# Kernel optimization log

Hardware: AMD Instinct MI355X
Metric: run time of the kernel (lower is better)

## Reference

```python
import jax, jax.numpy as jnp
import numpy as np

N, E, D, H, DH, FF, C, L = 50000, 640000, 128, 8, 16, 256, 5, 6
EPS = 1e-5


def _bn(x, g, b):
    # training-mode BatchNorm1d over the node dimension
    m = jnp.mean(x, axis=0)
    v = jnp.var(x, axis=0)
    return (x - m) * jax.lax.rsqrt(v + EPS) * g + b


def _sparse_mha(x, src, dst, Wq, Wk, Wv, Wo):
    # edge-restricted multi-head attention: softmax over incoming edges per dst node
    q = (x @ Wq).reshape(N, H, DH)
    k = (x @ Wk).reshape(N, H, DH)
    v = (x @ Wv).reshape(N, H, DH)
    s = jnp.einsum('ehd,ehd->eh', q[dst], k[src]) * (1.0 / np.sqrt(DH))  # [E,H]
    smax = jax.ops.segment_max(s, dst, num_segments=N)
    smax = jnp.where(jnp.isfinite(smax), smax, 0.0)  # guard isolated nodes
    e = jnp.exp(s - smax[dst])
    den = jax.ops.segment_sum(e, dst, num_segments=N)
    alpha = e / jnp.where(den > 0, den, 1.0)[dst]
    out = jax.ops.segment_sum(alpha[:, :, None] * v[src], dst, num_segments=N)  # [N,H,DH]
    return out.reshape(N, D) @ Wo


def setup_inputs() -> dict:
    key = jax.random.key(0)
    ks = jax.random.split(key, 18)
    f = lambda k, shp, sc: (jax.random.normal(k, shp, jnp.float32) * sc)
    return {
        'x': jax.random.normal(ks[0], (N, D), jnp.float32),
        'edge_index': jax.random.randint(ks[1], (2, E), 0, N),
        'Wq': f(ks[2], (L, D, D), 0.08),
        'Wk': f(ks[3], (L, D, D), 0.08),
        'Wv': f(ks[4], (L, D, D), 0.08),
        'Wo': f(ks[5], (L, D, D), 0.08),
        'g1': jnp.ones((L, D), jnp.float32),
        'bn1': jnp.zeros((L, D), jnp.float32),
        'W1': f(ks[6], (L, D, FF), 0.08),
        'bf1': jnp.zeros((L, FF), jnp.float32),
        'W2': f(ks[7], (L, FF, D), 0.06),
        'bf2': jnp.zeros((L, D), jnp.float32),
        'g2': jnp.ones((L, D), jnp.float32),
        'bn2': jnp.zeros((L, D), jnp.float32),
        'Wp': f(ks[8], (D, C), 0.08),
        'bp': jnp.zeros((C,), jnp.float32),
    }


def reference(x, edge_index, Wq, Wk, Wv, Wo, g1, bn1, W1, bf1, W2, bf2, g2, bn2, Wp, bp):
    src, dst = edge_index[0], edge_index[1]
    for i in range(L):  # fixed small layer count
        res = x  # residual is Identity (num_input == num_output)
        a = _sparse_mha(x, src, dst, Wq[i], Wk[i], Wv[i], Wo[i])
        x = _bn(a + res, g1[i], bn1[i])
        h = jax.nn.relu(x @ W1[i] + bf1[i])  # leakiness=0 -> relu
        x = _bn(x + (h @ W2[i] + bf2[i]), g2[i], bn2[i])
    node_pred = x @ Wp + bp
    return node_pred
```

## Files before the change

kernel.cpp:

```cpp
#include <hip/hip_runtime.h>
#include <hip/hip_bf16.h>
#include <cstdio>

#define NN 50000
#define EE 640000
#define DD 128
#define HH 8
#define DH 16
#define FFD 256
#define CC 5
#define LL 6
#define EPSV 1e-5f

typedef __attribute__((ext_vector_type(8))) short bf16x8;
typedef __attribute__((ext_vector_type(8))) unsigned short ushort8;
typedef __attribute__((ext_vector_type(4))) float f32x4;

__device__ __forceinline__ float bfu2f(unsigned short u) {
  union { unsigned int i; float f; } x; x.i = ((unsigned int)u) << 16; return x.f;
}
__device__ __forceinline__ unsigned short f2bf(float f) {
  union { float f; unsigned int i; } x; x.f = f;
  unsigned int r = (x.i + 0x7fffu + ((x.i >> 16) & 1u)) >> 16;
  return (unsigned short)r;
}

__global__ void detect_kernel(const unsigned int* __restrict__ g1w, int* __restrict__ flag) {
  if (threadIdx.x == 0 && blockIdx.x == 0) *flag = (g1w[0] == 0x3F803F80u) ? 1 : 0;
}

struct ConvJobs { const void* in[8]; float* out[8]; int n[8]; };
__global__ __launch_bounds__(256) void convert_batch_kernel(ConvJobs jobs, const int* __restrict__ flag) {
  int b = blockIdx.x;
  const void* in = jobs.in[b];
  float* out = jobs.out[b];
  int n = jobs.n[b];
  int use_bf = *flag;
  for (int i = threadIdx.x; i < n; i += 256) {
    if (use_bf) out[i] = bfu2f(((const unsigned short*)in)[i]);
    else        out[i] = ((const float*)in)[i];
  }
}

__global__ __launch_bounds__(256) void to_bf16_kernel(const void* __restrict__ in,
                                                      unsigned short* __restrict__ out, int n,
                                                      const int* __restrict__ flag) {
  int i = blockIdx.x * blockDim.x + threadIdx.x;
  if (i >= n) return;
  if (*flag) out[i] = ((const unsigned short*)in)[i];
  else       out[i] = f2bf(((const float*)in)[i]);
}

__global__ __launch_bounds__(256) void t_qkv_kernel(const void* __restrict__ wq, const void* __restrict__ wk,
                                                    const void* __restrict__ wv,
                                                    unsigned short* __restrict__ qkvT,
                                                    const int* __restrict__ flag) {
  int k = blockIdx.x, which = blockIdx.y, l = blockIdx.z;
  const void* in = (which == 0) ? wq : (which == 1) ? wk : wv;
  size_t off = (size_t)l * DD * DD;
  unsigned short* out = qkvT + (size_t)l * 384 * DD + (size_t)which * DD * DD;
  int use_bf = *flag;
  for (int n = threadIdx.x; n < DD; n += 256) {
    unsigned short v;
    if (use_bf) v = ((const unsigned short*)in)[off + (size_t)k * DD + n];
    else        v = f2bf(((const float*)in)[off + (size_t)k * DD + n]);
    out[(size_t)n * DD + k] = v;
  }
}

__global__ __launch_bounds__(256) void t_w_kernel(const void* __restrict__ in,
                                                  unsigned short* __restrict__ out,
                                                  int K, int N, const int* __restrict__ flag) {
  int k = blockIdx.x, l = blockIdx.y;
  size_t off = (size_t)l * K * N;
  unsigned short* o = out + (size_t)l * K * N;
  int use_bf = *flag;
  for (int n = threadIdx.x; n < N; n += 256) {
    unsigned short v;
    if (use_bf) v = ((const unsigned short*)in)[off + (size_t)k * N + n];
    else        v = f2bf(((const float*)in)[off + (size_t)k * N + n]);
    o[(size_t)n * K + k] = v;
  }
}

__global__ __launch_bounds__(256) void zero_kernel(int* __restrict__ p, int n) {
  int i = blockIdx.x * blockDim.x + threadIdx.x;
  if (i < n) p[i] = 0;
}

__global__ __launch_bounds__(256) void count_kernel(const int* __restrict__ dst, int* __restrict__ counts) {
  int e = blockIdx.x * blockDim.x + threadIdx.x;
  if (e < EE) atomicAdd(&counts[dst[e]], 1);
}

__global__ __launch_bounds__(256) void scan1_kernel(const int* __restrict__ counts,
                                                    int* __restrict__ row_ptr, int* __restrict__ partials) {
  __shared__ int sh[256];
  int t = threadIdx.x;
  int i = blockIdx.x * 256 + t;
  int v = (i < NN) ? counts[i] : 0;
  sh[t] = v; __syncthreads();
#pragma unroll
  for (int off = 1; off < 256; off <<= 1) {
    int u = (t >= off) ? sh[t - off] : 0;
    __syncthreads();
    sh[t] += u;
    __syncthreads();
  }
  if (i < NN) row_ptr[i] = sh[t] - v;
  if (t == 255) partials[blockIdx.x] = sh[t];
}

__global__ __launch_bounds__(256) void scan2_kernel(int* __restrict__ partials, int nb) {
  __shared__ int sh[256];
  int t = threadIdx.x;
  int v = (t < nb) ? partials[t] : 0;
  sh[t] = v; __syncthreads();
#pragma unroll
  for (int off = 1; off < 256; off <<= 1) {
    int u = (t >= off) ? sh[t - off] : 0;
    __syncthreads();
    sh[t] += u;
    __syncthreads();
  }
  if (t < nb) partials[t] = sh[t] - v;
}

__global__ __launch_bounds__(256) void scan3_kernel(int* __restrict__ row_ptr, const int* __restrict__ partials) {
  int i = blockIdx.x * 256 + threadIdx.x;
  if (i < NN) row_ptr[i] += partials[blockIdx.x];
  if (i == 0) row_ptr[NN] = EE;
}

__global__ __launch_bounds__(256) void fill_kernel(const int* __restrict__ src, const int* __restrict__ dst,
                                                   const int* __restrict__ row_ptr, int* __restrict__ cursor,
                                                   int* __restrict__ csr_src) {
  int e = blockIdx.x * blockDim.x + threadIdx.x;
  if (e < EE) {
    int d = dst[e];
    int pos = row_ptr[d] + atomicAdd(&cursor[d], 1);
    csr_src[pos] = src[e];
  }
}

template<int K, bool RELU, bool HASBIAS, bool HASRES, bool OUTBF, bool STATS>
__global__ __launch_bounds__(256) void mfma_gemm(const unsigned short* __restrict__ A,
                                                 const unsigned short* __restrict__ BT,
                                                 const float* __restrict__ bias,
                                                 const unsigned short* __restrict__ resid,
                                                 void* __restrict__ C, float* __restrict__ stats,
                                                 int M, int ldc) {
  __shared__ float lsum[64];
  __shared__ float lsq[64];
  int tid = threadIdx.x;
  int lane = tid & 63, wave = tid >> 6;
  int m0 = blockIdx.x * 128 + wave * 32;
  int n0 = blockIdx.y * 64;
  int lm = lane & 15;
  int quad = lane >> 4;
  int kq = quad * 8;

  int rowA[2];
#pragma unroll
  for (int r = 0; r < 2; r++) {
    int rr = m0 + 16 * r + lm;
    rowA[r] = (rr < M) ? rr : (M - 1);
  }
  const unsigned short* aptr0 = A + (size_t)rowA[0] * K + kq;
  const unsigned short* aptr1 = A + (size_t)rowA[1] * K + kq;
  const unsigned short* bptr[4];
#pragma unroll
  for (int c = 0; c < 4; c++)
    bptr[c] = BT + (size_t)(n0 + 16 * c + lm) * K + kq;

  f32x4 acc[2][4];
#pragma unroll
  for (int r = 0; r < 2; r++)
#pragma unroll
    for (int c = 0; c < 4; c++) acc[r][c] = (f32x4){0.f, 0.f, 0.f, 0.f};

#pragma unroll
  for (int kc = 0; kc < K; kc += 128) {
    bf16x8 a[2][4], b[4][4];
#pragma unroll
    for (int ks = 0; ks < 4; ks++) {
      a[0][ks] = *(const bf16x8*)(aptr0 + kc + ks * 32);
      a[1][ks] = *(const bf16x8*)(aptr1 + kc + ks * 32);
    }
#pragma unroll
    for (int c = 0; c < 4; c++)
#pragma unroll
      for (int ks = 0; ks < 4; ks++)
        b[c][ks] = *(const bf16x8*)(bptr[c] + kc + ks * 32);
#pragma unroll
    for (int ks = 0; ks < 4; ks++)
#pragma unroll
      for (int r = 0; r < 2; r++)
#pragma unroll
        for (int c = 0; c < 4; c++)
          acc[r][c] = __builtin_amdgcn_mfma_f32_16x16x32_bf16(b[c][ks], a[r][ks], acc[r][c], 0, 0, 0);
  }

  if (STATS) {
    if (tid < 64) { lsum[tid] = 0.f; lsq[tid] = 0.f; }
    __syncthreads();
  }

  float st_s[4][4], st_q[4][4];
  if (STATS) {
#pragma unroll
    for (int c = 0; c < 4; c++)
#pragma unroll
      for (int reg = 0; reg < 4; reg++) { st_s[c][reg] = 0.f; st_q[c][reg] = 0.f; }
  }

#pragma unroll
  for (int r = 0; r < 2; r++) {
    int row = m0 + 16 * r + lm;
    if (row >= M) continue;
#pragma unroll
    for (int c = 0; c < 4; c++) {
      int col = n0 + 16 * c + quad * 4;
      float4 bv = HASBIAS ? *(const float4*)(bias + col) : make_float4(0.f, 0.f, 0.f, 0.f);
      float o[4];
      o[0] = acc[r][c][0] + bv.x; o[1] = acc[r][c][1] + bv.y;
      o[2] = acc[r][c][2] + bv.z; o[3] = acc[r][c][3] + bv.w;
      if (HASRES) {
        ushort4 rr = *(const ushort4*)(resid + (size_t)row * ldc + col);
        o[0] += bfu2f(rr.x); o[1] += bfu2f(rr.y); o[2] += bfu2f(rr.z); o[3] += bfu2f(rr.w);
      }
      if (RELU) {
        o[0] = fmaxf(o[0], 0.f); o[1] = fmaxf(o[1], 0.f);
        o[2] = fmaxf(o[2], 0.f); o[3] = fmaxf(o[3], 0.f);
      }
      size_t idx = (size_t)row * ldc + col;
      if (OUTBF) {
        ushort4 w;
        w.x = f2bf(o[0]); w.y = f2bf(o[1]); w.z = f2bf(o[2]); w.w = f2bf(o[3]);
        *(ushort4*)((unsigned short*)C + idx) = w;
      } else {
        *(float4*)((float*)C + idx) = make_float4(o[0], o[1], o[2], o[3]);
      }
      if (STATS) {
#pragma unroll
        for (int reg = 0; reg < 4; reg++) {
          st_s[c][reg] += o[reg];
          st_q[c][reg] = fmaf(o[reg], o[reg], st_q[c][reg]);
        }
      }
    }
  }

  if (STATS) {
#pragma unroll
    for (int c = 0; c < 4; c++)
#pragma unroll
      for (int reg = 0; reg < 4; reg++) {
        float s = st_s[c][reg], q = st_q[c][reg];
        s += __shfl_xor(s, 1);  q += __shfl_xor(q, 1);
        s += __shfl_xor(s, 2);  q += __shfl_xor(q, 2);
        s += __shfl_xor(s, 4);  q += __shfl_xor(q, 4);
        s += __shfl_xor(s, 8);  q += __shfl_xor(q, 8);
        if (lm == 0) {
          atomicAdd(&lsum[16 * c + quad * 4 + reg], s);
          atomicAdd(&lsq[16 * c + quad * 4 + reg], q);
        }
      }
    __syncthreads();
    if (tid < 64) {
      atomicAdd(&stats[n0 + tid], lsum[tid]);
      atomicAdd(&stats[128 + n0 + tid], lsq[tid]);
    }
  }
}

__global__ __launch_bounds__(256) void attn_kernel(const unsigned short* __restrict__ qkv,
                                                   const int* __restrict__ row_ptr,
                                                   const int* __restrict__ csr_src,
                                                   unsigned short* __restrict__ t1) {
  int t = blockIdx.x * blockDim.x + threadIdx.x;
  int half = t & 1;
  int nh = t >> 1;
  int n = nh >> 3, h = nh & 7;
  const unsigned short* qp = qkv + (size_t)n * 384 + h * 16 + half * 8;
  float qf[8];
  {
    bf16x8 q0 = *(const bf16x8*)qp;
#pragma unroll
    for (int i = 0; i < 8; i++) qf[i] = bfu2f((unsigned short)q0[i]);
  }
  float m = -3.0e38f, l = 0.f;
  float A[8];
#pragma unroll
  for (int i = 0; i < 8; i++) A[i] = 0.f;
  int e0 = row_ptr[n], e1 = row_ptr[n + 1];
  if (e0 < e1) {
    int s = csr_src[e0];
    const unsigned short* kp = qkv + (size_t)s * 384 + 128 + h * 16 + half * 8;
    bf16x8 k0 = *(const bf16x8*)kp;
    bf16x8 v0 = *(const bf16x8*)(kp + 128);
    for (int e = e0; e < e1; e++) {
      int sn = csr_src[(e + 1 < e1) ? e + 1 : e];
      const unsigned short* kpn = qkv + (size_t)sn * 384 + 128 + h * 16 + half * 8;
      bf16x8 nk0 = *(const bf16x8*)kpn;
      bf16x8 nv0 = *(const bf16x8*)(kpn + 128);

      float part = 0.f;
#pragma unroll
      for (int i = 0; i < 8; i++) part += qf[i] * bfu2f((unsigned short)k0[i]);
      float sc = (part + __shfl_xor(part, 1)) * 0.25f;
      float mn = fmaxf(m, sc);
      float cf = __expf(m - mn);
      float p  = __expf(sc - mn);
      l = l * cf + p;
#pragma unroll
      for (int i = 0; i < 8; i++)
        A[i] = A[i] * cf + p * bfu2f((unsigned short)v0[i]);
      m = mn;
      k0 = nk0; v0 = nv0;
    }
  }
  float inv = (l > 0.f) ? 1.f / l : 0.f;
  ushort8 o0;
#pragma unroll
  for (int i = 0; i < 8; i++) o0[i] = f2bf(A[i] * inv);
  unsigned short* op = t1 + (size_t)n * 128 + h * 16 + half * 8;
  *(ushort8*)op = o0;
}

__global__ __launch_bounds__(256) void bn_apply_kernel(const float4* __restrict__ y4,
                                                       const float* __restrict__ statsL,
                                                       const float* __restrict__ g,
                                                       const float* __restrict__ b,
                                                       ushort4* __restrict__ xb) {
  __shared__ float ssc[128];
  __shared__ float ssh[128];
  int t = threadIdx.x;
  if (t < 128) {
    float mean = statsL[t] * (1.f / NN);
    float var  = statsL[128 + t] * (1.f / NN) - mean * mean;
    var = fmaxf(var, 0.f);
    float sc = g[t] * rsqrtf(var + EPSV);
    ssc[t] = sc;
    ssh[t] = b[t] - mean * sc;
  }
  __syncthreads();
  int i = blockIdx.x * 256 + t;
  const int total = NN * (DD / 4);
  if (i >= total) return;
  int c4 = (i & 31) * 4;
  float4 v = y4[i];
  ushort4 o;
  o.x = f2bf(fmaf(v.x, ssc[c4 + 0], ssh[c4 + 0]));
  o.y = f2bf(fmaf(v.y, ssc[c4 + 1], ssh[c4 + 1]));
  o.z = f2bf(fmaf(v.z, ssc[c4 + 2], ssh[c4 + 2]));
  o.w = f2bf(fmaf(v.w, ssc[c4 + 3], ssh[c4 + 3]));
  xb[i] = o;
}

__global__ __launch_bounds__(256) void proj_kernel(const unsigned short* __restrict__ x,
                                                   const float* __restrict__ Wp,
                                                   const float* __restrict__ bp,
                                                   void* __restrict__ out,
                                                   const int* __restrict__ flag) {
  __shared__ float W[DD * CC];
  __shared__ float bias[CC];
  for (int i = threadIdx.x; i < DD * CC; i += 256) W[i] = Wp[i];
  if (threadIdx.x < CC) bias[threadIdx.x] = bp[threadIdx.x];
  __syncthreads();
  int n = blockIdx.x * blockDim.x + threadIdx.x;
  if (n >= NN) return;
  float acc[CC];
#pragma unroll
  for (int c = 0; c < CC; c++) acc[c] = bias[c];
  const ushort4* xp = (const ushort4*)(x + (size_t)n * DD);
#pragma unroll
  for (int k4 = 0; k4 < DD / 4; k4++) {
    ushort4 u = xp[k4];
    float a0 = bfu2f(u.x), a1 = bfu2f(u.y), a2 = bfu2f(u.z), a3 = bfu2f(u.w);
    const float* w = &W[k4 * 4 * CC];
#pragma unroll
    for (int c = 0; c < CC; c++)
      acc[c] += a0 * w[c] + a1 * w[CC + c] + a2 * w[2 * CC + c] + a3 * w[3 * CC + c];
  }
  if (*flag) {
    __hip_bfloat16* o16 = (__hip_bfloat16*)out;
#pragma unroll
    for (int c = 0; c < CC; c++) o16[(size_t)n * CC + c] = __float2bfloat16(acc[c]);
  } else {
    float* o32 = (float*)out;
#pragma unroll
    for (int c = 0; c < CC; c++) o32[(size_t)n * CC + c] = acc[c];
  }
}

extern "C" void kernel_launch(void* const* d_in, const int* in_sizes, int n_in,
                              void* d_out, int out_size, void* d_ws, size_t ws_size,
                              hipStream_t stream) {
  const int* ei = (const int*)d_in[1];

  char* p = (char*)d_ws;
  auto carve = [&](size_t bytes) { char* r = p; p += (bytes + 255) & ~(size_t)255; return (void*)r; };
  unsigned short* xb   = (unsigned short*)carve((size_t)NN * DD * 2);
  unsigned short* qkv  = (unsigned short*)carve((size_t)NN * 384 * 2);
  unsigned short* t1   = (unsigned short*)carve((size_t)NN * DD * 2);
  unsigned short* hbuf = (unsigned short*)carve((size_t)NN * FFD * 2);
  float* y             = (float*)carve((size_t)NN * DD * 4);
  float* stats = (float*)carve(12 * 256 * 4);
  int* row_ptr = (int*)carve((size_t)(NN + 1) * 4);
  int* cursor  = (int*)carve((size_t)NN * 4);
  int* counts  = (int*)carve((size_t)NN * 4);
  int* csr_src = (int*)carve((size_t)EE * 4);
  int* flag    = (int*)carve(256);
  int* partials = (int*)carve(256 * 4);
  unsigned short* qkvT = (unsigned short*)carve((size_t)LL * 384 * DD * 2);
  unsigned short* WoT  = (unsigned short*)carve((size_t)LL * DD * DD * 2);
  unsigned short* W1T  = (unsigned short*)carve((size_t)LL * FFD * DD * 2);
  unsigned short* W2T  = (unsigned short*)carve((size_t)LL * DD * FFD * 2);
  float* g1_f  = (float*)carve((size_t)LL * DD * 4);
  float* bn1_f = (float*)carve((size_t)LL * DD * 4);
  float* bf1_f = (float*)carve((size_t)LL * FFD * 4);
  float* bf2_f = (float*)carve((size_t)LL * DD * 4);
  float* g2_f  = (float*)carve((size_t)LL * DD * 4);
  float* bn2_f = (float*)carve((size_t)LL * DD * 4);
  float* Wp_f  = (float*)carve((size_t)DD * CC * 4);
  float* bp_f  = (float*)carve((size_t)CC * 4);
  size_t need = (size_t)(p - (char*)d_ws);
  if (need > ws_size) {
    fprintf(stderr, "kernel_launch: workspace too small: need %zu, have %zu\n", need, ws_size);
    return;
  }

  const int* src  = ei;
  const int* dstp = ei + EE;

  detect_kernel<<<1, 64, 0, stream>>>((const unsigned int*)d_in[6], flag);
  to_bf16_kernel<<<(NN * DD + 255) / 256, 256, 0, stream>>>(d_in[0], xb, NN * DD, flag);

  {
    ConvJobs j;
    j.in[0] = d_in[6];  j.out[0] = g1_f;  j.n[0] = LL * DD;
    j.in[1] = d_in[7];  j.out[1] = bn1_f; j.n[1] = LL * DD;
    j.in[2] = d_in[9];  j.out[2] = bf1_f; j.n[2] = LL * FFD;
    j.in[3] = d_in[11]; j.out[3] = bf2_f; j.n[3] = LL * DD;
    j.in[4] = d_in[12]; j.out[4] = g2_f;  j.n[4] = LL * DD;
    j.in[5] = d_in[13]; j.out[5] = bn2_f; j.n[5] = LL * DD;
    j.in[6] = d_in[14]; j.out[6] = Wp_f;  j.n[6] = DD * CC;
    j.in[7] = d_in[15]; j.out[7] = bp_f;  j.n[7] = CC;
    convert_batch_kernel<<<8, 256, 0, stream>>>(j, flag);
  }

  t_qkv_kernel<<<dim3(DD, 3, LL), 256, 0, stream>>>(d_in[2], d_in[3], d_in[4], qkvT, flag);
  t_w_kernel<<<dim3(DD, LL), 256, 0, stream>>>(d_in[5], WoT, DD, DD, flag);
  t_w_kernel<<<dim3(DD, LL), 256, 0, stream>>>(d_in[8], W1T, DD, FFD, flag);
  t_w_kernel<<<dim3(FFD, LL), 256, 0, stream>>>(d_in[10], W2T, FFD, DD, flag);

  zero_kernel<<<12, 256, 0, stream>>>((int*)stats, 12 * 256);
  zero_kernel<<<(NN + 255) / 256, 256, 0, stream>>>(counts, NN);
  zero_kernel<<<(NN + 255) / 256, 256, 0, stream>>>(cursor, NN);

  const int NB = (NN + 255) / 256;
  count_kernel<<<(EE + 255) / 256, 256, 0, stream>>>(dstp, counts);
  scan1_kernel<<<NB, 256, 0, stream>>>(counts, row_ptr, partials);
  scan2_kernel<<<1, 256, 0, stream>>>(partials, NB);
  scan3_kernel<<<NB, 256, 0, stream>>>(row_ptr, partials);
  fill_kernel<<<(EE + 255) / 256, 256, 0, stream>>>(src, dstp, row_ptr, cursor, csr_src);

  const int gm = (NN + 127) / 128;
  for (int layer = 0; layer < LL; layer++) {
    const unsigned short* qkvT_l = qkvT + (size_t)layer * 384 * DD;
    const unsigned short* WoT_l  = WoT  + (size_t)layer * DD * DD;
    const unsigned short* W1T_l  = W1T  + (size_t)layer * FFD * DD;
    const unsigned short* W2T_l  = W2T  + (size_t)layer * DD * FFD;
    float* st1 = stats + (size_t)(layer * 2 + 0) * 256;
    float* st2 = stats + (size_t)(layer * 2 + 1) * 256;

    mfma_gemm<128, false, false, false, true, false><<<dim3(gm, 6), 256, 0, stream>>>(
        xb, qkvT_l, nullptr, nullptr, qkv, nullptr, NN, 384);
    attn_kernel<<<NN * HH * 2 / 256, 256, 0, stream>>>(qkv, row_ptr, csr_src, t1);
    mfma_gemm<128, false, false, true, false, true><<<dim3(gm, 2), 256, 0, stream>>>(
        t1, WoT_l, nullptr, xb, y, st1, NN, 128);
    bn_apply_kernel<<<(NN * 32 + 255) / 256, 256, 0, stream>>>(
        (const float4*)y, st1, g1_f + (size_t)layer * DD, bn1_f + (size_t)layer * DD, (ushort4*)xb);

    mfma_gemm<128, true, true, false, true, false><<<dim3(gm, 4), 256, 0, stream>>>(
        xb, W1T_l, bf1_f + (size_t)layer * FFD, nullptr, hbuf, nullptr, NN, 256);
    mfma_gemm<256, false, true, true, false, true><<<dim3(gm, 2), 256, 0, stream>>>(
        hbuf, W2T_l, bf2_f + (size_t)layer * DD, xb, y, st2, NN, 128);
    bn_apply_kernel<<<(NN * 32 + 255) / 256, 256, 0, stream>>>(
        (const float4*)y, st2, g2_f + (size_t)layer * DD, bn2_f + (size_t)layer * DD, (ushort4*)xb);
  }

  proj_kernel<<<(NN + 255) / 256, 256, 0, stream>>>(xb, Wp_f, bp_f, d_out, flag);
}
```

Baseline: 1.424 ms.

## Retile GEMM blocks, store pre-BN activations as bf16, tile weight transposes

GEMM blocks change from 128x64 to 64x128 tiles (2x2 waves), so the 128-wide outputs use one block column and BN stats reduce in one block per row tile. The k-loop now loads one 32-wide slice at a time instead of 128, which cuts register pressure but exposes less load-level parallelism. The pre-BN buffer y is stored as bf16 instead of fp32, halving its write and read traffic at some precision cost. Weight transposes use shared-memory 32x32 tiles for coalesced access.

```diff
diff --git a/kernel.cpp b/kernel.cpp
--- a/kernel.cpp
+++ b/kernel.cpp
@@ -51,35 +51,57 @@
   else       out[i] = f2bf(((const float*)in)[i]);
 }
 
-__global__ __launch_bounds__(256) void t_qkv_kernel(const void* __restrict__ wq, const void* __restrict__ wk,
-                                                    const void* __restrict__ wv,
-                                                    unsigned short* __restrict__ qkvT,
-                                                    const int* __restrict__ flag) {
-  int k = blockIdx.x, which = blockIdx.y, l = blockIdx.z;
+__global__ __launch_bounds__(256) void t_qkv_tiled(const void* __restrict__ wq, const void* __restrict__ wk,
+                                                   const void* __restrict__ wv,
+                                                   unsigned short* __restrict__ qkvT,
+                                                   const int* __restrict__ flag) {
+  __shared__ unsigned short tile[32][33];
+  int l = blockIdx.z / 3, which = blockIdx.z % 3;
   const void* in = (which == 0) ? wq : (which == 1) ? wk : wv;
   size_t off = (size_t)l * DD * DD;
   unsigned short* out = qkvT + (size_t)l * 384 * DD + (size_t)which * DD * DD;
+  int tx = threadIdx.x & 31, ty = threadIdx.x >> 5;
+  int k0 = blockIdx.x * 32, n0 = blockIdx.y * 32;
   int use_bf = *flag;
-  for (int n = threadIdx.x; n < DD; n += 256) {
+#pragma unroll
+  for (int i = 0; i < 4; i++) {
+    int k = k0 + ty + i * 8;
     unsigned short v;
-    if (use_bf) v = ((const unsigned short*)in)[off + (size_t)k * DD + n];
-    else        v = f2bf(((const float*)in)[off + (size_t)k * DD + n]);
-    out[(size_t)n * DD + k] = v;
-  }
-}
-
-__global__ __launch_bounds__(256) void t_w_kernel(const void* __restrict__ in,
-                                                  unsigned short* __restrict__ out,
-                                                  int K, int N, const int* __restrict__ flag) {
-  int k = blockIdx.x, l = blockIdx.y;
+    if (use_bf) v = ((const unsigned short*)in)[off + (size_t)k * DD + n0 + tx];
+    else        v = f2bf(((const float*)in)[off + (size_t)k * DD + n0 + tx]);
+    tile[ty + i * 8][tx] = v;
+  }
+  __syncthreads();
+#pragma unroll
+  for (int i = 0; i < 4; i++) {
+    int n = n0 + ty + i * 8;
+    out[(size_t)n * DD + k0 + tx] = tile[tx][ty + i * 8];
+  }
+}
+
+__global__ __launch_bounds__(256) void t_w_tiled(const void* __restrict__ in,
+                                                 unsigned short* __restrict__ out,
+                                                 int K, int N, const int* __restrict__ flag) {
+  __shared__ unsigned short tile[32][33];
+  int l = blockIdx.z;
   size_t off = (size_t)l * K * N;
   unsigned short* o = out + (size_t)l * K * N;
+  int tx = threadIdx.x & 31, ty = threadIdx.x >> 5;
+  int k0 = blockIdx.x * 32, n0 = blockIdx.y * 32;
   int use_bf = *flag;
-  for (int n = threadIdx.x; n < N; n += 256) {
+#pragma unroll
+  for (int i = 0; i < 4; i++) {
+    int k = k0 + ty + i * 8;
     unsigned short v;
-    if (use_bf) v = ((const unsigned short*)in)[off + (size_t)k * N + n];
-    else        v = f2bf(((const float*)in)[off + (size_t)k * N + n]);
-    o[(size_t)n * K + k] = v;
+    if (use_bf) v = ((const unsigned short*)in)[off + (size_t)k * N + n0 + tx];
+    else        v = f2bf(((const float*)in)[off + (size_t)k * N + n0 + tx]);
+    tile[ty + i * 8][tx] = v;
+  }
+  __syncthreads();
+#pragma unroll
+  for (int i = 0; i < 4; i++) {
+    int n = n0 + ty + i * 8;
+    o[(size_t)n * K + k0 + tx] = tile[tx][ty + i * 8];
   }
 }
 
@@ -150,12 +172,12 @@
                                                  const unsigned short* __restrict__ resid,
                                                  void* __restrict__ C, float* __restrict__ stats,
                                                  int M, int ldc) {
-  __shared__ float lsum[64];
-  __shared__ float lsq[64];
+  __shared__ float lsum[128];
+  __shared__ float lsq[128];
   int tid = threadIdx.x;
   int lane = tid & 63, wave = tid >> 6;
-  int m0 = blockIdx.x * 128 + wave * 32;
-  int n0 = blockIdx.y * 64;
+  int m0 = blockIdx.x * 64 + (wave >> 1) * 32;
+  int n0 = blockIdx.y * 128 + (wave & 1) * 64;
   int lm = lane & 15;
   int quad = lane >> 4;
   int kq = quad * 8;
@@ -180,29 +202,22 @@
     for (int c = 0; c < 4; c++) acc[r][c] = (f32x4){0.f, 0.f, 0.f, 0.f};
 
 #pragma unroll
-  for (int kc = 0; kc < K; kc += 128) {
-    bf16x8 a[2][4], b[4][4];
-#pragma unroll
-    for (int ks = 0; ks < 4; ks++) {
-      a[0][ks] = *(const bf16x8*)(aptr0 + kc + ks * 32);
-      a[1][ks] = *(const bf16x8*)(aptr1 + kc + ks * 32);
-    }
+  for (int k0 = 0; k0 < K; k0 += 32) {
+    bf16x8 a[2], b[4];
+    a[0] = *(const bf16x8*)(aptr0 + k0);
+    a[1] = *(const bf16x8*)(aptr1 + k0);
 #pragma unroll
     for (int c = 0; c < 4; c++)
-#pragma unroll
-      for (int ks = 0; ks < 4; ks++)
-        b[c][ks] = *(const bf16x8*)(bptr[c] + kc + ks * 32);
-#pragma unroll
-    for (int ks = 0; ks < 4; ks++)
-#pragma unroll
-      for (int r = 0; r < 2; r++)
-#pragma unroll
-        for (int c = 0; c < 4; c++)
-          acc[r][c] = __builtin_amdgcn_mfma_f32_16x16x32_bf16(b[c][ks], a[r][ks], acc[r][c], 0, 0, 0);
+      b[c] = *(const bf16x8*)(bptr[c] + k0);
+#pragma unroll
+    for (int r = 0; r < 2; r++)
+#pragma unroll
+      for (int c = 0; c < 4; c++)
+        acc[r][c] = __builtin_amdgcn_mfma_f32_16x16x32_bf16(b[c], a[r], acc[r][c], 0, 0, 0);
   }
 
   if (STATS) {
-    if (tid < 64) { lsum[tid] = 0.f; lsq[tid] = 0.f; }
+    if (tid < 128) { lsum[tid] = 0.f; lsq[tid] = 0.f; }
     __syncthreads();
   }
 
@@ -262,14 +277,15 @@
         s += __shfl_xor(s, 4);  q += __shfl_xor(q, 4);
         s += __shfl_xor(s, 8);  q += __shfl_xor(q, 8);
         if (lm == 0) {
-          atomicAdd(&lsum[16 * c + quad * 4 + reg], s);
-          atomicAdd(&lsq[16 * c + quad * 4 + reg], q);
+          int cl = (wave & 1) * 64 + 16 * c + quad * 4 + reg;
+          atomicAdd(&lsum[cl], s);
+          atomicAdd(&lsq[cl], q);
         }
       }
     __syncthreads();
-    if (tid < 64) {
-      atomicAdd(&stats[n0 + tid], lsum[tid]);
-      atomicAdd(&stats[128 + n0 + tid], lsq[tid]);
+    if (tid < 128) {
+      atomicAdd(&stats[tid], lsum[tid]);
+      atomicAdd(&stats[128 + tid], lsq[tid]);
     }
   }
 }
@@ -328,7 +344,7 @@
   *(ushort8*)op = o0;
 }
 
-__global__ __launch_bounds__(256) void bn_apply_kernel(const float4* __restrict__ y4,
+__global__ __launch_bounds__(256) void bn_apply_kernel(const ushort4* __restrict__ y4,
                                                        const float* __restrict__ statsL,
                                                        const float* __restrict__ g,
                                                        const float* __restrict__ b,
@@ -349,12 +365,12 @@
   const int total = NN * (DD / 4);
   if (i >= total) return;
   int c4 = (i & 31) * 4;
-  float4 v = y4[i];
+  ushort4 v = y4[i];
   ushort4 o;
-  o.x = f2bf(fmaf(v.x, ssc[c4 + 0], ssh[c4 + 0]));
-  o.y = f2bf(fmaf(v.y, ssc[c4 + 1], ssh[c4 + 1]));
-  o.z = f2bf(fmaf(v.z, ssc[c4 + 2], ssh[c4 + 2]));
-  o.w = f2bf(fmaf(v.w, ssc[c4 + 3], ssh[c4 + 3]));
+  o.x = f2bf(fmaf(bfu2f(v.x), ssc[c4 + 0], ssh[c4 + 0]));
+  o.y = f2bf(fmaf(bfu2f(v.y), ssc[c4 + 1], ssh[c4 + 1]));
+  o.z = f2bf(fmaf(bfu2f(v.z), ssc[c4 + 2], ssh[c4 + 2]));
+  o.w = f2bf(fmaf(bfu2f(v.w), ssc[c4 + 3], ssh[c4 + 3]));
   xb[i] = o;
 }
 
@@ -405,7 +421,7 @@
   unsigned short* qkv  = (unsigned short*)carve((size_t)NN * 384 * 2);
   unsigned short* t1   = (unsigned short*)carve((size_t)NN * DD * 2);
   unsigned short* hbuf = (unsigned short*)carve((size_t)NN * FFD * 2);
-  float* y             = (float*)carve((size_t)NN * DD * 4);
+  unsigned short* y    = (unsigned short*)carve((size_t)NN * DD * 2);
   float* stats = (float*)carve(12 * 256 * 4);
   int* row_ptr = (int*)carve((size_t)(NN + 1) * 4);
   int* cursor  = (int*)carve((size_t)NN * 4);
@@ -450,10 +466,10 @@
     convert_batch_kernel<<<8, 256, 0, stream>>>(j, flag);
   }
 
-  t_qkv_kernel<<<dim3(DD, 3, LL), 256, 0, stream>>>(d_in[2], d_in[3], d_in[4], qkvT, flag);
-  t_w_kernel<<<dim3(DD, LL), 256, 0, stream>>>(d_in[5], WoT, DD, DD, flag);
-  t_w_kernel<<<dim3(DD, LL), 256, 0, stream>>>(d_in[8], W1T, DD, FFD, flag);
-  t_w_kernel<<<dim3(FFD, LL), 256, 0, stream>>>(d_in[10], W2T, FFD, DD, flag);
+  t_qkv_tiled<<<dim3(4, 4, 3 * LL), 256, 0, stream>>>(d_in[2], d_in[3], d_in[4], qkvT, flag);
+  t_w_tiled<<<dim3(4, 4, LL), 256, 0, stream>>>(d_in[5], WoT, DD, DD, flag);
+  t_w_tiled<<<dim3(4, 8, LL), 256, 0, stream>>>(d_in[8], W1T, DD, FFD, flag);
+  t_w_tiled<<<dim3(8, 4, LL), 256, 0, stream>>>(d_in[10], W2T, FFD, DD, flag);
 
   zero_kernel<<<12, 256, 0, stream>>>((int*)stats, 12 * 256);
   zero_kernel<<<(NN + 255) / 256, 256, 0, stream>>>(counts, NN);
@@ -466,7 +482,7 @@
   scan3_kernel<<<NB, 256, 0, stream>>>(row_ptr, partials);
   fill_kernel<<<(EE + 255) / 256, 256, 0, stream>>>(src, dstp, row_ptr, cursor, csr_src);
 
-  const int gm = (NN + 127) / 128;
+  const int gm = (NN + 63) / 64;
   for (int layer = 0; layer < LL; layer++) {
     const unsigned short* qkvT_l = qkvT + (size_t)layer * 384 * DD;
     const unsigned short* WoT_l  = WoT  + (size_t)layer * DD * DD;
@@ -475,20 +491,20 @@
     float* st1 = stats + (size_t)(layer * 2 + 0) * 256;
     float* st2 = stats + (size_t)(layer * 2 + 1) * 256;
 
-    mfma_gemm<128, false, false, false, true, false><<<dim3(gm, 6), 256, 0, stream>>>(
+    mfma_gemm<128, false, false, false, true, false><<<dim3(gm, 3), 256, 0, stream>>>(
         xb, qkvT_l, nullptr, nullptr, qkv, nullptr, NN, 384);
     attn_kernel<<<NN * HH * 2 / 256, 256, 0, stream>>>(qkv, row_ptr, csr_src, t1);
-    mfma_gemm<128, false, false, true, false, true><<<dim3(gm, 2), 256, 0, stream>>>(
+    mfma_gemm<128, false, false, true, true, true><<<dim3(gm, 1), 256, 0, stream>>>(
         t1, WoT_l, nullptr, xb, y, st1, NN, 128);
     bn_apply_kernel<<<(NN * 32 + 255) / 256, 256, 0, stream>>>(
-        (const float4*)y, st1, g1_f + (size_t)layer * DD, bn1_f + (size_t)layer * DD, (ushort4*)xb);
-
-    mfma_gemm<128, true, true, false, true, false><<<dim3(gm, 4), 256, 0, stream>>>(
+        (const ushort4*)y, st1, g1_f + (size_t)layer * DD, bn1_f + (size_t)layer * DD, (ushort4*)xb);
+
+    mfma_gemm<128, true, true, false, true, false><<<dim3(gm, 2), 256, 0, stream>>>(
         xb, W1T_l, bf1_f + (size_t)layer * FFD, nullptr, hbuf, nullptr, NN, 256);
-    mfma_gemm<256, false, true, true, false, true><<<dim3(gm, 2), 256, 0, stream>>>(
+    mfma_gemm<256, false, true, true, true, true><<<dim3(gm, 1), 256, 0, stream>>>(
         hbuf, W2T_l, bf2_f + (size_t)layer * DD, xb, y, st2, NN, 128);
     bn_apply_kernel<<<(NN * 32 + 255) / 256, 256, 0, stream>>>(
-        (const float4*)y, st2, g2_f + (size_t)layer * DD, bn2_f + (size_t)layer * DD, (ushort4*)xb);
+        (const ushort4*)y, st2, g2_f + (size_t)layer * DD, bn2_f + (size_t)layer * DD, (ushort4*)xb);
   }
 
   proj_kernel<<<(NN + 255) / 256, 256, 0, stream>>>(xb, Wp_f, bp_f, d_out, flag);
```

New measurement: 1.485 ms. +4.3%, slower.
